# Optimization experiments

Hardware: AMD Instinct MI355X
Metric: run time of the kernel (lower is better)

Reference implementation:

```python
import jax, jax.numpy as jnp
import numpy as np

B, K, H, W, N = 256, 16, 64, 64, 1024   # batch, channels (n_ch), grid H/W, sampled sites
F_IN = 9 * K - 1                         # 3x3 neighborhood * K channels, minus center channel


def setup_inputs() -> dict:
    key = jax.random.key(0)
    ks = jax.random.split(key, 8)
    z_int = jax.random.randint(ks[0], (B, K, H, W), 0, 16, dtype=jnp.int32)
    bs = jax.random.randint(ks[1], (N,), 0, K, dtype=jnp.int32)
    ii = jax.random.randint(ks[2], (N,), 0, H, dtype=jnp.int32)
    jj = jax.random.randint(ks[3], (N,), 0, W, dtype=jnp.int32)
    W1 = jax.random.normal(ks[4], (F_IN, 128), dtype=jnp.float32) * 0.05
    b1 = jnp.zeros((128,), dtype=jnp.float32)
    W2 = jax.random.normal(ks[5], (128, 16), dtype=jnp.float32) * 0.05
    b2 = jnp.zeros((16,), dtype=jnp.float32)
    return {"z_int": z_int, "bs": bs, "ii": ii, "jj": jj,
            "W1": W1, "b1": b1, "W2": W2, "b2": b2}


def _gather_ctx(z_f, bs, ii, jj):
    # Faithful to get_context ordering: loops di, dj (each in [-1,0,1]) then b,
    # skipping (di==0, dj==0, b==bi). Flattened skip position = 4*K + bi.
    off = jnp.array([-1, 0, 1], dtype=jnp.int32)
    di = jnp.repeat(off, 3)          # [9]
    dj = jnp.tile(off, 3)            # [9]
    ni = (ii[:, None] + di[None, :]) % H   # [N, 9] toroidal wrap
    nj = (jj[:, None] + dj[None, :]) % W   # [N, 9]
    ctx = z_f[:, :, ni, nj]                # [B, K, N, 9]
    ctx = jnp.transpose(ctx, (2, 0, 3, 1)).reshape(N, B, 9 * K)  # [N, B, 9K], (di,dj) major then b
    drop = 4 * K + bs                      # [N] center-channel flat index
    idx = jnp.arange(F_IN, dtype=jnp.int32)
    keep = idx[None, :] + (idx[None, :] >= drop[:, None]).astype(jnp.int32)  # [N, F_IN]
    return jax.vmap(lambda c, k: c[:, k])(ctx, keep)  # [N, B, F_IN]


def reference(z_int, bs, ii, jj, W1, b1, W2, b2):
    z_f = z_int.astype(jnp.float32) / 15.0
    ctx = _gather_ctx(z_f, bs, ii, jj)                 # [N, B, 9K-1]
    h = jax.nn.relu(jnp.einsum('nbf,fh->nbh', ctx, W1) + b1)
    logits = jnp.einsum('nbh,hc->nbc', h, W2) + b2     # [N, B, 16]
    pred = jnp.argmax(logits, axis=-1)                 # [N, B]
    tgt = z_int[:, bs, ii, jj].T                       # [N, B]
    rate = jnp.mean((pred != tgt).astype(jnp.float32)) # np.mean of per-site mean == global mean
    return rate
```

## Files before the change

### kernel.cpp

```cpp
#include <hip/hip_runtime.h>
#include <stdint.h>

#define NB 1024
#define BB 256
#define KK 16
#define HH 64
#define WW 64
#define F_FULL 144
#define HDIM 128
#define CDIM 16
#define KPAD 160
#define APITCH 168
#define HPITCH 136
#define ABYTES (64 * APITCH * 2)
#define NCTR 128

typedef __bf16 bf16x8 __attribute__((ext_vector_type(8)));
typedef float f32x4 __attribute__((ext_vector_type(4)));

#define W1T_OFF 1024
#define W1T_BYTES (16 * HDIM * KPAD * 2)
#define W2B_OFF (W1T_OFF + W1T_BYTES)
#define W2B_BYTES (CDIM * HDIM * 2)
#define ZT_OFF (W2B_OFF + W2B_BYTES)

__device__ __forceinline__ unsigned short bf16_bits(float v) {
    __bf16 b = (__bf16)v;
    return __builtin_bit_cast(unsigned short, b);
}

#define TP 144
__global__ __launch_bounds__(256) void prep_kernel(
    const int* __restrict__ z, const float* __restrict__ W1,
    const float* __restrict__ W2, uint8_t* __restrict__ zt,
    unsigned short* __restrict__ W1t, unsigned short* __restrict__ W2b,
    int* __restrict__ counters) {
    int bid = blockIdx.x;
    int t = threadIdx.x;
    if (bid < 4096) {
        __shared__ uint8_t tile[32 * TP];
        int bx = bid & 127;
        int by = bid >> 7;
        int c0 = bx * 32, r0 = by * 128;
#pragma unroll
        for (int i = 0; i < 4; ++i) {
            int lin = i * 256 + t;
            int c = lin & 31;
            int rq = lin >> 5;
            uchar4 v;
            v.x = (uint8_t)z[(size_t)(r0 + rq * 4 + 0) * 4096 + c0 + c];
            v.y = (uint8_t)z[(size_t)(r0 + rq * 4 + 1) * 4096 + c0 + c];
            v.z = (uint8_t)z[(size_t)(r0 + rq * 4 + 2) * 4096 + c0 + c];
            v.w = (uint8_t)z[(size_t)(r0 + rq * 4 + 3) * 4096 + c0 + c];
            *(uchar4*)(tile + c * TP + rq * 4) = v;
        }
        __syncthreads();
        int cy = t >> 3, rx = t & 7;
        uint4 v = *(const uint4*)(tile + cy * TP + rx * 16);
        *(uint4*)(zt + (size_t)(c0 + cy) * 4096 + r0 + rx * 16) = v;
    } else if (bid < 5376) {
        int idx = (bid - 4096) * 256 + t;
        int k = idx % KPAD;
        int h = (idx / KPAD) % HDIM;
        int s = idx / (KPAD * HDIM);
        int drop = 4 * KK + s;
        float val = 0.0f;
        if (k < F_FULL && k != drop) {
            int src = k - (k > drop ? 1 : 0);
            val = W1[src * HDIM + h];
        }
        W1t[idx] = bf16_bits(val);
    } else {
        int idx = (bid - 5376) * 256 + t;
        if (idx < CDIM * HDIM) {
            int k = idx % HDIM;
            int c = idx / HDIM;
            W2b[idx] = bf16_bits(W2[k * CDIM + c]);
        }
        if (bid == 5376 && t < NCTR) counters[t] = 0;
    }
}

__global__ __launch_bounds__(256, 3) void main_kernel(
    const uint8_t* __restrict__ zt, const unsigned short* __restrict__ W1t,
    const float* __restrict__ b1, const unsigned short* __restrict__ W2b,
    const float* __restrict__ b2, const int* __restrict__ bs,
    const int* __restrict__ ii, const int* __restrict__ jj,
    int* __restrict__ counters) {
    __shared__ __align__(16) unsigned char smem[2 * ABYTES + 1024];
    unsigned short* sA0 = (unsigned short*)smem;
    unsigned short* sA1 = (unsigned short*)(smem + ABYTES);

    int t = threadIdx.x;
    int n = blockIdx.x;
    int wave = t >> 6, lane = t & 63;
    int l15 = lane & 15, l4 = lane >> 4;

    int in_ = ii[n], jn = jj[n], sn = bs[n];

    {
        const uint8_t* src = zt + ((size_t)n << 14) + t * 16;
#pragma unroll
        for (int k = 0; k < 4; ++k)
            __builtin_amdgcn_global_load_lds(
                (const __attribute__((address_space(1))) void*)(src + (k << 12)),
                (__attribute__((address_space(3))) void*)(smem + 2 * ABYTES), 16, 0, 0);
    }

    int p0 = t >> 6;
    int ni0 = (in_ + p0 / 3 - 1) & (HH - 1);
    int nj0 = (jn + p0 % 3 - 1) & (WW - 1);
    size_t base0 = ((size_t)(ni0 * WW + nj0) * BB) << 4;
    int p1 = p0 + 4;
    int ni1 = (in_ + p1 / 3 - 1) & (HH - 1);
    int nj1 = (jn + p1 % 3 - 1) & (WW - 1);
    size_t base1 = ((size_t)(ni1 * WW + nj1) * BB) << 4;
    int ni2 = (in_ + 1) & (HH - 1);
    int nj2 = (jn + 1) & (WW - 1);
    size_t base2 = ((size_t)(ni2 * WW + nj2) * BB) << 4;

    uint4 ga[4], gb[4], gc[4];
#pragma unroll
    for (int tl = 0; tl < 3; ++tl) {
        size_t boff = (size_t)((t & 63) + tl * 64) << 4;
        ga[tl] = *(const uint4*)(zt + base0 + boff);
        gb[tl] = *(const uint4*)(zt + base1 + boff);
        if (t < 64) gc[tl] = *(const uint4*)(zt + base2 + boff);
    }

    const unsigned short* w1s = W1t + (size_t)sn * (HDIM * KPAD);
    int n0 = wave * 32;
    bf16x8 Bf[2][5];
#pragma unroll
    for (int nt = 0; nt < 2; ++nt)
#pragma unroll
        for (int ks = 0; ks < 5; ++ks)
            Bf[nt][ks] = *(const bf16x8*)(w1s + (n0 + nt * 16 + l15) * KPAD + ks * 32 + l4 * 8);
    bf16x8 Bf2[4];
#pragma unroll
    for (int ks = 0; ks < 4; ++ks)
        Bf2[ks] = *(const bf16x8*)(W2b + l15 * HDIM + ks * 32 + l4 * 8);
    float b1v0 = b1[n0 + l15], b1v1 = b1[n0 + 16 + l15];
    float b2v = b2[l15];

    if (t < 192) {
        int b = t / 3, part = t % 3;
        *(uint4*)(sA0 + b * APITCH + F_FULL + part * 8) = make_uint4(0, 0, 0, 0);
        *(uint4*)(sA1 + b * APITCH + F_FULL + part * 8) = make_uint4(0, 0, 0, 0);
    }

    auto gwrite = [&](uint4 A, uint4 B, uint4 C, unsigned short* dst) {
        int b = t & 63;
        auto conv = [&](uint4 raw, int p) {
            const uint8_t* bytes = (const uint8_t*)&raw;
            union { __bf16 h[16]; uint4 q[2]; } u;
#pragma unroll
            for (int k = 0; k < 16; ++k)
                u.h[k] = (__bf16)((float)bytes[k] * (1.0f / 15.0f));
            uint4* d = (uint4*)(dst + b * APITCH + p * 16);
            d[0] = u.q[0];
            d[1] = u.q[1];
        };
        conv(A, p0);
        conv(B, p0 + 4);
        if (t < 64) conv(C, 8);
    };

    gwrite(ga[0], gb[0], gc[0], sA0);

    int err = 0;
    size_t tbase = ((size_t)(in_ * WW + jn) * BB) << 4;

    for (int tile = 0; tile < 4; ++tile) {
        unsigned short* sA = (tile & 1) ? sA1 : sA0;
        unsigned short* sH = sA;
        __syncthreads();

        f32x4 acc[4][2] = {};
#pragma unroll
        for (int mt = 0; mt < 4; ++mt) {
            bf16x8 Af[5];
#pragma unroll
            for (int ks = 0; ks < 5; ++ks)
                Af[ks] = *(const bf16x8*)(sA + (mt * 16 + l15) * APITCH + ks * 32 + l4 * 8);
#pragma unroll
            for (int ks = 0; ks < 5; ++ks) {
                acc[mt][0] = __builtin_amdgcn_mfma_f32_16x16x32_bf16(Af[ks], Bf[0][ks], acc[mt][0], 0, 0, 0);
                acc[mt][1] = __builtin_amdgcn_mfma_f32_16x16x32_bf16(Af[ks], Bf[1][ks], acc[mt][1], 0, 0, 0);
            }
        }
        __syncthreads();

#pragma unroll
        for (int mt = 0; mt < 4; ++mt)
#pragma unroll
            for (int nt = 0; nt < 2; ++nt) {
                float bv = nt ? b1v1 : b1v0;
                int hcol = n0 + nt * 16 + l15;
#pragma unroll
                for (int r = 0; r < 4; ++r) {
                    int b = mt * 16 + l4 * 4 + r;
                    float v = fmaxf(acc[mt][nt][r] + bv, 0.0f);
                    sH[b * HPITCH + hcol] = bf16_bits(v);
                }
            }
        __syncthreads();

        f32x4 acc2 = {};
#pragma unroll
        for (int ks = 0; ks < 4; ++ks) {
            bf16x8 Af = *(const bf16x8*)(sH + (wave * 16 + l15) * HPITCH + ks * 32 + l4 * 8);
            acc2 = __builtin_amdgcn_mfma_f32_16x16x32_bf16(Af, Bf2[ks], acc2, 0, 0, 0);
        }

#pragma unroll
        for (int r = 0; r < 4; ++r) {
            float v = acc2[r] + b2v;
            int idx = l15;
#pragma unroll
            for (int m = 1; m < 16; m <<= 1) {
                float ov = __shfl_xor(v, m);
                int oi = __shfl_xor(idx, m);
                if (ov > v || (ov == v && oi < idx)) { v = ov; idx = oi; }
            }
            int bg = tile * 64 + wave * 16 + l4 * 4 + r;
            int tgt = zt[tbase + ((size_t)bg << 4) + sn];
            unsigned long long mm = __ballot(l15 == 0 && idx != tgt);
            err += (int)__popcll(mm);
        }

        if (tile == 0) {
            gwrite(ga[1], gb[1], gc[1], sA1);
            size_t boff = (size_t)((t & 63) + 192) << 4;
            ga[3] = *(const uint4*)(zt + base0 + boff);
            gb[3] = *(const uint4*)(zt + base1 + boff);
            if (t < 64) gc[3] = *(const uint4*)(zt + base2 + boff);
        } else if (tile == 1) {
            gwrite(ga[2], gb[2], gc[2], sA0);
        } else if (tile == 2) {
            gwrite(ga[3], gb[3], gc[3], sA1);
        }
    }

    if (lane == 0) atomicAdd(&counters[n & (NCTR - 1)], err);
}

__global__ void finalize_kernel(const int* __restrict__ counters, float* __restrict__ out) {
    int t = threadIdx.x;
    int s = counters[t] + counters[t + 64];
#pragma unroll
    for (int m = 32; m; m >>= 1) s += __shfl_down(s, m);
    if (t == 0) out[0] = (float)s / (float)(NB * BB);
}

extern "C" void kernel_launch(void* const* d_in, const int* in_sizes, int n_in,
                              void* d_out, int out_size, void* d_ws, size_t ws_size,
                              hipStream_t stream) {
    const int* z = (const int*)d_in[0];
    const int* bs = (const int*)d_in[1];
    const int* ii = (const int*)d_in[2];
    const int* jj = (const int*)d_in[3];
    const float* W1 = (const float*)d_in[4];
    const float* b1 = (const float*)d_in[5];
    const float* W2 = (const float*)d_in[6];
    const float* b2 = (const float*)d_in[7];
    float* out = (float*)d_out;

    uint8_t* ws = (uint8_t*)d_ws;
    int* counters = (int*)ws;
    unsigned short* W1t = (unsigned short*)(ws + W1T_OFF);
    unsigned short* W2b = (unsigned short*)(ws + W2B_OFF);
    uint8_t* zt = ws + ZT_OFF;

    prep_kernel<<<5384, 256, 0, stream>>>(z, W1, W2, zt, W1t, W2b, counters);
    main_kernel<<<NB, 256, 0, stream>>>(zt, W1t, b1, W2b, b2, bs, ii, jj, counters);
    finalize_kernel<<<1, 1 * 64, 0, stream>>>(counters, out);
}
```

Baseline: 145.0 us.

## Vectorize z transpose prep, shrink LDS, and pipeline tile loads for higher occupancy

The prep transpose now processes 128x128 tiles with 16-byte vectorized int loads packed into 32-bit words, using fewer blocks. The main kernel drops the unused global_load_lds prefetch and its extra LDS, trims A pitch to 160, holds only two register slots of gathered data (loading tiles 2 and 3 mid-loop), and reloads W2 fragments per use to cut registers. Launch bounds go from 3 to 4 blocks per CU. The risks are LDS bank conflicts from the unpadded pitch, plus extra global loads of W2 and less latency hiding for the deferred gathers.

```diff
diff --git a/kernel.cpp b/kernel.cpp
--- a/kernel.cpp
+++ b/kernel.cpp
@@ -10,7 +10,7 @@
 #define HDIM 128
 #define CDIM 16
 #define KPAD 160
-#define APITCH 168
+#define APITCH 160
 #define HPITCH 136
 #define ABYTES (64 * APITCH * 2)
 #define NCTR 128
@@ -29,7 +29,7 @@
     return __builtin_bit_cast(unsigned short, b);
 }
 
-#define TP 144
+#define TPW 33
 __global__ __launch_bounds__(256) void prep_kernel(
     const int* __restrict__ z, const float* __restrict__ W1,
     const float* __restrict__ W2, uint8_t* __restrict__ zt,
@@ -37,29 +37,47 @@
     int* __restrict__ counters) {
     int bid = blockIdx.x;
     int t = threadIdx.x;
-    if (bid < 4096) {
-        __shared__ uint8_t tile[32 * TP];
-        int bx = bid & 127;
-        int by = bid >> 7;
-        int c0 = bx * 32, r0 = by * 128;
+    if (bid < 1024) {
+        __shared__ uint32_t tile[128 * TPW];
+        int bx = bid & 31;
+        int by = bid >> 5;
+        int c0 = bx * 128, r0 = by * 128;
+        int rq = t >> 3;
+        int cq = t & 7;
+        uint4 v[4][4];
+#pragma unroll
+        for (int jr = 0; jr < 4; ++jr) {
+            const int* zp = z + (size_t)(r0 + rq * 4 + jr) * 4096 + c0 + cq * 16;
+#pragma unroll
+            for (int jc = 0; jc < 4; ++jc)
+                v[jr][jc] = *(const uint4*)(zp + jc * 4);
+        }
+#pragma unroll
+        for (int jc = 0; jc < 4; ++jc) {
+            uint32_t w0 = v[0][jc].x | (v[1][jc].x << 8) | (v[2][jc].x << 16) | (v[3][jc].x << 24);
+            uint32_t w1 = v[0][jc].y | (v[1][jc].y << 8) | (v[2][jc].y << 16) | (v[3][jc].y << 24);
+            uint32_t w2 = v[0][jc].z | (v[1][jc].z << 8) | (v[2][jc].z << 16) | (v[3][jc].z << 24);
+            uint32_t w3 = v[0][jc].w | (v[1][jc].w << 8) | (v[2][jc].w << 16) | (v[3][jc].w << 24);
+            int cb = cq * 16 + jc * 4;
+            tile[(cb + 0) * TPW + rq] = w0;
+            tile[(cb + 1) * TPW + rq] = w1;
+            tile[(cb + 2) * TPW + rq] = w2;
+            tile[(cb + 3) * TPW + rq] = w3;
+        }
+        __syncthreads();
 #pragma unroll
         for (int i = 0; i < 4; ++i) {
-            int lin = i * 256 + t;
-            int c = lin & 31;
-            int rq = lin >> 5;
-            uchar4 v;
-            v.x = (uint8_t)z[(size_t)(r0 + rq * 4 + 0) * 4096 + c0 + c];
-            v.y = (uint8_t)z[(size_t)(r0 + rq * 4 + 1) * 4096 + c0 + c];
-            v.z = (uint8_t)z[(size_t)(r0 + rq * 4 + 2) * 4096 + c0 + c];
-            v.w = (uint8_t)z[(size_t)(r0 + rq * 4 + 3) * 4096 + c0 + c];
-            *(uchar4*)(tile + c * TP + rq * 4) = v;
-        }
-        __syncthreads();
-        int cy = t >> 3, rx = t & 7;
-        uint4 v = *(const uint4*)(tile + cy * TP + rx * 16);
-        *(uint4*)(zt + (size_t)(c0 + cy) * 4096 + r0 + rx * 16) = v;
-    } else if (bid < 5376) {
-        int idx = (bid - 4096) * 256 + t;
+            int m = i * 256 + t;
+            int c = m >> 3, rx = m & 7;
+            uint4 o;
+            o.x = tile[c * TPW + rx * 4 + 0];
+            o.y = tile[c * TPW + rx * 4 + 1];
+            o.z = tile[c * TPW + rx * 4 + 2];
+            o.w = tile[c * TPW + rx * 4 + 3];
+            *(uint4*)(zt + (size_t)(c0 + c) * 4096 + r0 + rx * 16) = o;
+        }
+    } else if (bid < 2304) {
+        int idx = (bid - 1024) * 256 + t;
         int k = idx % KPAD;
         int h = (idx / KPAD) % HDIM;
         int s = idx / (KPAD * HDIM);
@@ -71,23 +89,23 @@
         }
         W1t[idx] = bf16_bits(val);
     } else {
-        int idx = (bid - 5376) * 256 + t;
+        int idx = (bid - 2304) * 256 + t;
         if (idx < CDIM * HDIM) {
             int k = idx % HDIM;
             int c = idx / HDIM;
             W2b[idx] = bf16_bits(W2[k * CDIM + c]);
         }
-        if (bid == 5376 && t < NCTR) counters[t] = 0;
+        if (bid == 2304 && t < NCTR) counters[t] = 0;
     }
 }
 
-__global__ __launch_bounds__(256, 3) void main_kernel(
+__global__ __launch_bounds__(256, 4) void main_kernel(
     const uint8_t* __restrict__ zt, const unsigned short* __restrict__ W1t,
     const float* __restrict__ b1, const unsigned short* __restrict__ W2b,
     const float* __restrict__ b2, const int* __restrict__ bs,
     const int* __restrict__ ii, const int* __restrict__ jj,
     int* __restrict__ counters) {
-    __shared__ __align__(16) unsigned char smem[2 * ABYTES + 1024];
+    __shared__ __align__(16) unsigned char smem[2 * ABYTES];
     unsigned short* sA0 = (unsigned short*)smem;
     unsigned short* sA1 = (unsigned short*)(smem + ABYTES);
 
@@ -97,15 +115,6 @@
     int l15 = lane & 15, l4 = lane >> 4;
 
     int in_ = ii[n], jn = jj[n], sn = bs[n];
-
-    {
-        const uint8_t* src = zt + ((size_t)n << 14) + t * 16;
-#pragma unroll
-        for (int k = 0; k < 4; ++k)
-            __builtin_amdgcn_global_load_lds(
-                (const __attribute__((address_space(1))) void*)(src + (k << 12)),
-                (__attribute__((address_space(3))) void*)(smem + 2 * ABYTES), 16, 0, 0);
-    }
 
     int p0 = t >> 6;
     int ni0 = (in_ + p0 / 3 - 1) & (HH - 1);
@@ -119,14 +128,16 @@
     int nj2 = (jn + 1) & (WW - 1);
     size_t base2 = ((size_t)(ni2 * WW + nj2) * BB) << 4;
 
-    uint4 ga[4], gb[4], gc[4];
-#pragma unroll
-    for (int tl = 0; tl < 3; ++tl) {
-        size_t boff = (size_t)((t & 63) + tl * 64) << 4;
-        ga[tl] = *(const uint4*)(zt + base0 + boff);
-        gb[tl] = *(const uint4*)(zt + base1 + boff);
-        if (t < 64) gc[tl] = *(const uint4*)(zt + base2 + boff);
-    }
+    uint4 ga[2], gb[2], gc[2];
+    auto gload = [&](int slot, int tile) {
+        size_t boff = (size_t)((t & 63) + tile * 64) << 4;
+        ga[slot] = *(const uint4*)(zt + base0 + boff);
+        gb[slot] = *(const uint4*)(zt + base1 + boff);
+        if (t < 64) gc[slot] = *(const uint4*)(zt + base2 + boff);
+    };
+
+    gload(0, 0);
+    gload(1, 1);
 
     const unsigned short* w1s = W1t + (size_t)sn * (HDIM * KPAD);
     int n0 = wave * 32;
@@ -136,20 +147,16 @@
 #pragma unroll
         for (int ks = 0; ks < 5; ++ks)
             Bf[nt][ks] = *(const bf16x8*)(w1s + (n0 + nt * 16 + l15) * KPAD + ks * 32 + l4 * 8);
-    bf16x8 Bf2[4];
-#pragma unroll
-    for (int ks = 0; ks < 4; ++ks)
-        Bf2[ks] = *(const bf16x8*)(W2b + l15 * HDIM + ks * 32 + l4 * 8);
     float b1v0 = b1[n0 + l15], b1v1 = b1[n0 + 16 + l15];
     float b2v = b2[l15];
 
-    if (t < 192) {
-        int b = t / 3, part = t % 3;
+    if (t < 128) {
+        int b = t >> 1, part = t & 1;
         *(uint4*)(sA0 + b * APITCH + F_FULL + part * 8) = make_uint4(0, 0, 0, 0);
         *(uint4*)(sA1 + b * APITCH + F_FULL + part * 8) = make_uint4(0, 0, 0, 0);
     }
 
-    auto gwrite = [&](uint4 A, uint4 B, uint4 C, unsigned short* dst) {
+    auto gwrite = [&](int slot, unsigned short* dst) {
         int b = t & 63;
         auto conv = [&](uint4 raw, int p) {
             const uint8_t* bytes = (const uint8_t*)&raw;
@@ -161,12 +168,12 @@
             d[0] = u.q[0];
             d[1] = u.q[1];
         };
-        conv(A, p0);
-        conv(B, p0 + 4);
-        if (t < 64) conv(C, 8);
+        conv(ga[slot], p0);
+        conv(gb[slot], p0 + 4);
+        if (t < 64) conv(gc[slot], 8);
     };
 
-    gwrite(ga[0], gb[0], gc[0], sA0);
+    gwrite(0, sA0);
 
     int err = 0;
     size_t tbase = ((size_t)(in_ * WW + jn) * BB) << 4;
@@ -190,6 +197,8 @@
             }
         }
         __syncthreads();
+
+        if (tile < 2) gload(tile & 1, tile + 2);
 
 #pragma unroll
         for (int mt = 0; mt < 4; ++mt)
@@ -209,8 +218,9 @@
         f32x4 acc2 = {};
 #pragma unroll
         for (int ks = 0; ks < 4; ++ks) {
+            bf16x8 Bf2 = *(const bf16x8*)(W2b + l15 * HDIM + ks * 32 + l4 * 8);
             bf16x8 Af = *(const bf16x8*)(sH + (wave * 16 + l15) * HPITCH + ks * 32 + l4 * 8);
-            acc2 = __builtin_amdgcn_mfma_f32_16x16x32_bf16(Af, Bf2[ks], acc2, 0, 0, 0);
+            acc2 = __builtin_amdgcn_mfma_f32_16x16x32_bf16(Af, Bf2, acc2, 0, 0, 0);
         }
 
 #pragma unroll
@@ -229,17 +239,7 @@
             err += (int)__popcll(mm);
         }
 
-        if (tile == 0) {
-            gwrite(ga[1], gb[1], gc[1], sA1);
-            size_t boff = (size_t)((t & 63) + 192) << 4;
-            ga[3] = *(const uint4*)(zt + base0 + boff);
-            gb[3] = *(const uint4*)(zt + base1 + boff);
-            if (t < 64) gc[3] = *(const uint4*)(zt + base2 + boff);
-        } else if (tile == 1) {
-            gwrite(ga[2], gb[2], gc[2], sA0);
-        } else if (tile == 2) {
-            gwrite(ga[3], gb[3], gc[3], sA1);
-        }
+        if (tile < 3) gwrite((tile + 1) & 1, (tile & 1) ? sA0 : sA1);
     }
 
     if (lane == 0) atomicAdd(&counters[n & (NCTR - 1)], err);
@@ -272,7 +272,7 @@
     unsigned short* W2b = (unsigned short*)(ws + W2B_OFF);
     uint8_t* zt = ws + ZT_OFF;
 
-    prep_kernel<<<5384, 256, 0, stream>>>(z, W1, W2, zt, W1t, W2b, counters);
+    prep_kernel<<<2312, 256, 0, stream>>>(z, W1, W2, zt, W1t, W2b, counters);
     main_kernel<<<NB, 256, 0, stream>>>(zt, W1t, b1, W2b, b2, bs, ii, jj, counters);
-    finalize_kernel<<<1, 1 * 64, 0, stream>>>(counters, out);
-}
+    finalize_kernel<<<1, 64, 0, stream>>>(counters, out);
+}
```

Measured after the change: 151.0 us. 4.1% more time.
